# Kernel optimization log

Measured on AMD Instinct MI355X. Metric: run time of the kernel, lower is better.

## Reference

```python
import jax, jax.numpy as jnp
import numpy as np

NUM_FEATURES = 81   # atom feature width used in matmuls
N_NODES = 262144
N_COLS = 103        # num_features + num_bond
OUT_CH = 128
COORD = 3           # distance rule slice [0:3]


def setup_inputs() -> dict:
    key = jax.random.key(0)
    k1, k2, k3, k4 = jax.random.split(key, 4)
    features = jax.random.normal(k1, (N_NODES, N_COLS), dtype=jnp.float32)
    # columns 81, 82 hold neighbor indices (0 => no neighbor), stored as floats
    idx = jax.random.randint(k4, (N_NODES, 2), 0, N_NODES).astype(jnp.float32)
    features = features.at[:, NUM_FEATURES:NUM_FEATURES + 2].set(idx)
    w_s = jax.random.normal(k2, (NUM_FEATURES, OUT_CH), dtype=jnp.float32) * 0.05
    w_n = jax.random.normal(k3, (N_COLS, OUT_CH), dtype=jnp.float32) * 0.05
    return {"features": features, "w_s": w_s, "w_n": w_n}


def reference(features, w_s, w_n):
    F = NUM_FEATURES
    self_f = features[:, :F]                       # [N, F]
    new_features = self_f @ w_s                    # [N, C] self term

    idx0 = features[:, F].astype(jnp.int32)        # neighbor slot 0
    idx1 = features[:, F + 1].astype(jnp.int32)    # neighbor slot 1

    def neighbor_contrib(idx):
        nei = features[idx]                                        # gather [N, 103]
        # rule 0: 'distance' over [0:COORD] -> keep neighbor slice, record distance
        d = jnp.sqrt(jnp.sum(jnp.square(self_f[:, :COORD] - nei[:, :COORD]), axis=-1))
        seg_dist = nei[:, :COORD]                                  # [N, 3]
        # rule 1: 'sum' over [COORD:F]
        seg_sum = self_f[:, COORD:F] + nei[:, COORD:F]             # [N, F-3]
        comb = jnp.concatenate([seg_dist, seg_sum], axis=-1)       # [N, F]
        d_eff = jnp.where(d > 0, d, jnp.float32(0.01))
        comb = comb / jnp.square(d_eff)[:, None]                   # distance scaling
        return comb @ w_n[:F] + new_features                       # tiny-matmul batched

    c0 = neighbor_contrib(idx0)
    c1 = neighbor_contrib(idx1)
    # rows with no valid neighbor were never written -> zeros
    out = jnp.where((idx1 != 0)[:, None], c1,
                    jnp.where((idx0 != 0)[:, None], c0, jnp.float32(0.0)))
    return out
```

## Files before the change

### kernel.cpp

```cpp
#include <hip/hip_runtime.h>
#include <hip/hip_bf16.h>

constexpr int kNodes = 262144;
constexpr int NC  = 103;
constexpr int F   = 81;
constexpr int OC  = 128;
constexpr int NKS = 6;
constexpr int THREADS = 256;

typedef __attribute__((ext_vector_type(8))) short bf16x8;
typedef __attribute__((ext_vector_type(4))) float f32x4;

__device__ inline ushort f2bf(float f) {
  uint u = __float_as_uint(f);
  return (ushort)((u + 0x7fffu + ((u >> 16) & 1u)) >> 16);
}

__global__ __launch_bounds__(256)
void prep_w(const float* __restrict__ w_s, const float* __restrict__ w_n,
            ushort* __restrict__ wf) {
  int t = blockIdx.x * 256 + threadIdx.x;
  if (t >= NKS * 8 * 64) return;
  int l  = t & 63;
  int ct = (t >> 6) & 7;
  int ks = t >> 9;
  int c  = ct * 16 + (l & 15);
  int kb = ks * 32 + ((l >> 4) << 3);
  union { ushort u[8]; int4 v; } o;
  #pragma unroll
  for (int i = 0; i < 8; ++i) {
    int k = kb + i;
    float f = 0.f;
    if (k < F)                      f = w_s[k * OC + c];
    else if (k >= 96 && k < 96 + F) f = w_n[(k - 96) * OC + c];
    o.u[i] = f2bf(f);
  }
  ((int4*)wf)[t] = o.v;
}

__device__ inline short bfc(float x) {
  return (short)__bfloat16_as_ushort(__float2bfloat16(x));
}

__global__ __launch_bounds__(THREADS, 2)
void rgc_flat(const float* __restrict__ feat, const ushort* __restrict__ wf,
              float* __restrict__ out) {
  const int tid  = threadIdx.x;
  const int l    = tid & 63;
  const int q    = l >> 4;
  const int lrow = l & 15;
  const int off0 = q * 8;
  const long tbase = (long)(blockIdx.x * 4 + (tid >> 6)) * 16;
  const float* srow = feat + (tbase + lrow) * NC;
  const bf16x8* wfv = (const bf16x8*)wf;

  float pidx0 = srow[F];
  float pidx1 = srow[F + 1];
  float sc0 = srow[0], sc1 = srow[1], sc2 = srow[2];
  float s[24];
  #pragma unroll
  for (int c = 0; c < 3; ++c)
    #pragma unroll
    for (int i = 0; i < 8; ++i)
      s[c * 8 + i] = srow[c * 32 + off0 + i];

  bf16x8 bcur[8], bnxt[8];
  #pragma unroll
  for (int ct = 0; ct < 8; ++ct) bcur[ct] = wfv[ct * 64 + l];

  int i0 = (int)pidx0, i1 = (int)pidx1;
  int sel = (i1 != 0) ? i1 : i0;
  float alive = (i1 != 0 || i0 != 0) ? 1.f : 0.f;
  const float* nrow = feat + (long)sel * NC;
  float nc0 = nrow[0], nc1 = nrow[1], nc2 = nrow[2];
  float n[24];
  #pragma unroll
  for (int c = 0; c < 3; ++c)
    #pragma unroll
    for (int i = 0; i < 8; ++i)
      n[c * 8 + i] = nrow[c * 32 + off0 + i];

  float dx = sc0 - nc0, dy = sc1 - nc1, dz = sc2 - nc2;
  float d2 = dx * dx + dy * dy + dz * dz;
  float cs = alive * ((d2 > 0.f) ? (1.f / d2) : 10000.f);

  bf16x8 afS[3], afC[3];
  #pragma unroll
  for (int c = 0; c < 3; ++c) {
    #pragma unroll
    for (int i = 0; i < 8; ++i) {
      float sv = s[c * 8 + i];
      float nv = n[c * 8 + i];
      afS[c][i] = bfc(sv * alive);
      float se = sv;
      if (c == 0 && i < 3) se = (q == 0) ? 0.f : sv;
      afC[c][i] = bfc((nv + se) * cs);
    }
  }

  f32x4 acc[8];
  #pragma unroll
  for (int i = 0; i < 8; ++i) acc[i] = (f32x4)(0.f);

  #pragma unroll
  for (int ks = 0; ks < NKS; ++ks) {
    if (ks + 1 < NKS) {
      #pragma unroll
      for (int ct = 0; ct < 8; ++ct) bnxt[ct] = wfv[((ks + 1) * 8 + ct) * 64 + l];
    }
    bf16x8 af = (ks < 3) ? afS[ks] : afC[ks - 3];
    #pragma unroll
    for (int ct = 0; ct < 8; ++ct)
      acc[ct] = __builtin_amdgcn_mfma_f32_16x16x32_bf16(af, bcur[ct], acc[ct], 0, 0, 0);
    #pragma unroll
    for (int ct = 0; ct < 8; ++ct) bcur[ct] = bnxt[ct];
  }

  const long orow = tbase + q * 4;
  const int  col  = l & 15;
  #pragma unroll
  for (int ct = 0; ct < 8; ++ct) {
    #pragma unroll
    for (int r = 0; r < 4; ++r) {
      out[(orow + r) * OC + ct * 16 + col] = acc[ct][r];
    }
  }
}

extern "C" void kernel_launch(void* const* d_in, const int* in_sizes, int n_in,
                              void* d_out, int out_size, void* d_ws, size_t ws_size,
                              hipStream_t stream) {
  const float* feat = (const float*)d_in[0];
  const float* w_s  = (const float*)d_in[1];
  const float* w_n  = (const float*)d_in[2];
  float* outp = (float*)d_out;
  ushort* wf = (ushort*)d_ws;

  prep_w<<<dim3((NKS * 8 * 64 + 255) / 256), 256, 0, stream>>>(w_s, w_n, wf);
  rgc_flat<<<dim3(kNodes / 64), THREADS, 0, stream>>>(feat, wf, outp);
}
```

Measured before the change: 79.11 us.

## Process 32 rows per wave, reusing weight fragments across two row tiles

```diff
diff --git a/kernel.cpp b/kernel.cpp
--- a/kernel.cpp
+++ b/kernel.cpp
@@ -10,6 +10,7 @@
 
 typedef __attribute__((ext_vector_type(8))) short bf16x8;
 typedef __attribute__((ext_vector_type(4))) float f32x4;
+typedef __attribute__((ext_vector_type(8))) float f32x8;
 
 __device__ inline ushort f2bf(float f) {
   uint u = __float_as_uint(f);
@@ -42,87 +43,113 @@
   return (short)__bfloat16_as_ushort(__float2bfloat16(x));
 }
 
-__global__ __launch_bounds__(THREADS, 2)
-void rgc_flat(const float* __restrict__ feat, const ushort* __restrict__ wf,
-              float* __restrict__ out) {
+#define LOAD8(dst, p, base)                 \
+  {                                         \
+    _Pragma("unroll")                       \
+    for (int _i = 0; _i < 8; ++_i) (dst)[_i] = (p)[(base) + _i]; \
+  }
+
+__global__ __launch_bounds__(THREADS)
+void rgc_flat32(const float* __restrict__ feat, const ushort* __restrict__ wf,
+                float* __restrict__ out) {
   const int tid  = threadIdx.x;
   const int l    = tid & 63;
   const int q    = l >> 4;
   const int lrow = l & 15;
   const int off0 = q * 8;
-  const long tbase = (long)(blockIdx.x * 4 + (tid >> 6)) * 16;
-  const float* srow = feat + (tbase + lrow) * NC;
+  const long wbase = (long)(blockIdx.x * 4 + (tid >> 6)) * 32;
+  const float* srowA = feat + (wbase + lrow) * NC;
+  const float* srowB = feat + (wbase + 16 + lrow) * NC;
   const bf16x8* wfv = (const bf16x8*)wf;
 
-  float pidx0 = srow[F];
-  float pidx1 = srow[F + 1];
-  float sc0 = srow[0], sc1 = srow[1], sc2 = srow[2];
-  float s[24];
-  #pragma unroll
-  for (int c = 0; c < 3; ++c)
+  f32x8 vA0, vA1, vA2, vB0, vB1, vB2;
+  LOAD8(vA0, srowA, off0); LOAD8(vA1, srowA, 32 + off0); LOAD8(vA2, srowA, 64 + off0);
+  LOAD8(vB0, srowB, off0); LOAD8(vB1, srowB, 32 + off0); LOAD8(vB2, srowB, 64 + off0);
+  float iA0 = srowA[F], iA1 = srowA[F + 1];
+  float iB0 = srowB[F], iB1 = srowB[F + 1];
+  float cA0 = srowA[0], cA1 = srowA[1], cA2 = srowA[2];
+  float cB0 = srowB[0], cB1 = srowB[1], cB2 = srowB[2];
+  asm volatile("" :: "v"(vA0), "v"(vA1), "v"(vA2), "v"(vB0), "v"(vB1), "v"(vB2));
+
+  int selA; float aliveA;
+  { int i0 = (int)iA0, i1 = (int)iA1;
+    selA = (i1 != 0) ? i1 : i0; aliveA = (i1 != 0 || i0 != 0) ? 1.f : 0.f; }
+  int selB; float aliveB;
+  { int i0 = (int)iB0, i1 = (int)iB1;
+    selB = (i1 != 0) ? i1 : i0; aliveB = (i1 != 0 || i0 != 0) ? 1.f : 0.f; }
+  const float* nrowA = feat + (long)selA * NC;
+  const float* nrowB = feat + (long)selB * NC;
+
+  f32x8 wA0, wA1, wA2, wB0, wB1, wB2;
+  LOAD8(wA0, nrowA, off0); LOAD8(wA1, nrowA, 32 + off0); LOAD8(wA2, nrowA, 64 + off0);
+  LOAD8(wB0, nrowB, off0); LOAD8(wB1, nrowB, 32 + off0); LOAD8(wB2, nrowB, 64 + off0);
+  float nA0 = nrowA[0], nA1 = nrowA[1], nA2 = nrowA[2];
+  float nB0 = nrowB[0], nB1 = nrowB[1], nB2 = nrowB[2];
+  asm volatile("" :: "v"(wA0), "v"(wA1), "v"(wA2), "v"(wB0), "v"(wB1), "v"(wB2));
+
+  float dxA = cA0 - nA0, dyA = cA1 - nA1, dzA = cA2 - nA2;
+  float d2A = dxA * dxA + dyA * dyA + dzA * dzA;
+  float csA = aliveA * ((d2A > 0.f) ? (1.f / d2A) : 10000.f);
+  float dxB = cB0 - nB0, dyB = cB1 - nB1, dzB = cB2 - nB2;
+  float d2B = dxB * dxB + dyB * dyB + dzB * dzB;
+  float csB = aliveB * ((d2B > 0.f) ? (1.f / d2B) : 10000.f);
+
+  bf16x8 fSA[3], fCA[3], fSB[3], fCB[3];
+  {
+    const f32x8 sA[3] = {vA0, vA1, vA2}, sB[3] = {vB0, vB1, vB2};
+    const f32x8 nA[3] = {wA0, wA1, wA2}, nB[3] = {wB0, wB1, wB2};
     #pragma unroll
-    for (int i = 0; i < 8; ++i)
-      s[c * 8 + i] = srow[c * 32 + off0 + i];
-
-  bf16x8 bcur[8], bnxt[8];
-  #pragma unroll
-  for (int ct = 0; ct < 8; ++ct) bcur[ct] = wfv[ct * 64 + l];
-
-  int i0 = (int)pidx0, i1 = (int)pidx1;
-  int sel = (i1 != 0) ? i1 : i0;
-  float alive = (i1 != 0 || i0 != 0) ? 1.f : 0.f;
-  const float* nrow = feat + (long)sel * NC;
-  float nc0 = nrow[0], nc1 = nrow[1], nc2 = nrow[2];
-  float n[24];
-  #pragma unroll
-  for (int c = 0; c < 3; ++c)
-    #pragma unroll
-    for (int i = 0; i < 8; ++i)
-      n[c * 8 + i] = nrow[c * 32 + off0 + i];
-
-  float dx = sc0 - nc0, dy = sc1 - nc1, dz = sc2 - nc2;
-  float d2 = dx * dx + dy * dy + dz * dz;
-  float cs = alive * ((d2 > 0.f) ? (1.f / d2) : 10000.f);
-
-  bf16x8 afS[3], afC[3];
-  #pragma unroll
-  for (int c = 0; c < 3; ++c) {
-    #pragma unroll
-    for (int i = 0; i < 8; ++i) {
-      float sv = s[c * 8 + i];
-      float nv = n[c * 8 + i];
-      afS[c][i] = bfc(sv * alive);
-      float se = sv;
-      if (c == 0 && i < 3) se = (q == 0) ? 0.f : sv;
-      afC[c][i] = bfc((nv + se) * cs);
+    for (int c = 0; c < 3; ++c) {
+      #pragma unroll
+      for (int i = 0; i < 8; ++i) {
+        float svA = sA[c][i], nvA = nA[c][i];
+        float svB = sB[c][i], nvB = nB[c][i];
+        fSA[c][i] = bfc(svA * aliveA);
+        fSB[c][i] = bfc(svB * aliveB);
+        float seA = svA, seB = svB;
+        if (c == 0 && i < 3 && q == 0) { seA = 0.f; seB = 0.f; }
+        fCA[c][i] = bfc((nvA + seA) * csA);
+        fCB[c][i] = bfc((nvB + seB) * csB);
+      }
     }
   }
 
-  f32x4 acc[8];
+  const int col = l & 15;
   #pragma unroll
-  for (int i = 0; i < 8; ++i) acc[i] = (f32x4)(0.f);
+  for (int h = 0; h < 2; ++h) {
+    f32x4 accA[4], accB[4];
+    #pragma unroll
+    for (int j = 0; j < 4; ++j) { accA[j] = (f32x4)(0.f); accB[j] = (f32x4)(0.f); }
 
-  #pragma unroll
-  for (int ks = 0; ks < NKS; ++ks) {
-    if (ks + 1 < NKS) {
+    bf16x8 bc[4], bn[4];
+    #pragma unroll
+    for (int j = 0; j < 4; ++j) bc[j] = wfv[(h * 4 + j) * 64 + l];
+
+    #pragma unroll
+    for (int ks = 0; ks < NKS; ++ks) {
+      if (ks + 1 < NKS) {
+        #pragma unroll
+        for (int j = 0; j < 4; ++j) bn[j] = wfv[((ks + 1) * 8 + h * 4 + j) * 64 + l];
+      }
+      bf16x8 afA = (ks < 3) ? fSA[ks] : fCA[ks - 3];
+      bf16x8 afB = (ks < 3) ? fSB[ks] : fCB[ks - 3];
       #pragma unroll
-      for (int ct = 0; ct < 8; ++ct) bnxt[ct] = wfv[((ks + 1) * 8 + ct) * 64 + l];
+      for (int j = 0; j < 4; ++j) {
+        accA[j] = __builtin_amdgcn_mfma_f32_16x16x32_bf16(afA, bc[j], accA[j], 0, 0, 0);
+        accB[j] = __builtin_amdgcn_mfma_f32_16x16x32_bf16(afB, bc[j], accB[j], 0, 0, 0);
+      }
+      #pragma unroll
+      for (int j = 0; j < 4; ++j) bc[j] = bn[j];
     }
-    bf16x8 af = (ks < 3) ? afS[ks] : afC[ks - 3];
+
     #pragma unroll
-    for (int ct = 0; ct < 8; ++ct)
-      acc[ct] = __builtin_amdgcn_mfma_f32_16x16x32_bf16(af, bcur[ct], acc[ct], 0, 0, 0);
-    #pragma unroll
-    for (int ct = 0; ct < 8; ++ct) bcur[ct] = bnxt[ct];
-  }
-
-  const long orow = tbase + q * 4;
-  const int  col  = l & 15;
-  #pragma unroll
-  for (int ct = 0; ct < 8; ++ct) {
-    #pragma unroll
-    for (int r = 0; r < 4; ++r) {
-      out[(orow + r) * OC + ct * 16 + col] = acc[ct][r];
+    for (int j = 0; j < 4; ++j) {
+      const int ct = h * 4 + j;
+      #pragma unroll
+      for (int r = 0; r < 4; ++r) {
+        out[(wbase + q * 4 + r) * OC + ct * 16 + col]      = accA[j][r];
+        out[(wbase + 16 + q * 4 + r) * OC + ct * 16 + col] = accB[j][r];
+      }
     }
   }
 }
@@ -137,5 +164,5 @@
   ushort* wf = (ushort*)d_ws;
 
   prep_w<<<dim3((NKS * 8 * 64 + 255) / 256), 256, 0, stream>>>(w_s, w_n, wf);
-  rgc_flat<<<dim3(kNodes / 64), THREADS, 0, stream>>>(feat, wf, outp);
+  rgc_flat32<<<dim3(kNodes / 128), THREADS, 0, stream>>>(feat, wf, outp);
 }
```

Result: faster. 68.52 us (-13.4%).

## Stage self and neighbor rows in LDS with coalesced loads, split output columns across waves

Applied to the files above, without the earlier changes.

```diff
diff --git a/kernel.cpp b/kernel.cpp
--- a/kernel.cpp
+++ b/kernel.cpp
@@ -6,7 +6,10 @@
 constexpr int F   = 81;
 constexpr int OC  = 128;
 constexpr int NKS = 6;
+constexpr int NPB = 64;
 constexpr int THREADS = 256;
+constexpr int NEI_STRIDE = 100;
+constexpr int GW = 96;
 
 typedef __attribute__((ext_vector_type(8))) short bf16x8;
 typedef __attribute__((ext_vector_type(4))) float f32x4;
@@ -14,6 +17,10 @@
 __device__ inline ushort f2bf(float f) {
   uint u = __float_as_uint(f);
   return (ushort)((u + 0x7fffu + ((u >> 16) & 1u)) >> 16);
+}
+
+__device__ inline short bfc(float x) {
+  return (short)__bfloat16_as_ushort(__float2bfloat16(x));
 }
 
 __global__ __launch_bounds__(256)
@@ -38,91 +45,105 @@
   ((int4*)wf)[t] = o.v;
 }
 
-__device__ inline short bfc(float x) {
-  return (short)__bfloat16_as_ushort(__float2bfloat16(x));
-}
+__global__ __launch_bounds__(THREADS)
+void rgc_v8(const float* __restrict__ feat, const ushort* __restrict__ wf,
+            float* __restrict__ out) {
+  __shared__ float lds_self[NPB * NC];
+  __shared__ float lds_nei[NPB * NEI_STRIDE];
+  __shared__ int   s_sel[NPB];
+  __shared__ float s_alive[NPB];
+  __shared__ float s_cs[NPB];
 
-__global__ __launch_bounds__(THREADS, 2)
-void rgc_flat(const float* __restrict__ feat, const ushort* __restrict__ wf,
-              float* __restrict__ out) {
-  const int tid  = threadIdx.x;
-  const int l    = tid & 63;
+  const int tid = threadIdx.x;
+  const int w   = tid >> 6;
+  const int l   = tid & 63;
+  const long base = (long)blockIdx.x * NPB;
+  const float* fbase = feat + base * NC;
+
+  const bf16x8* wfv = (const bf16x8*)wf;
+  bf16x8 bA[NKS], bB[NKS];
+  #pragma unroll
+  for (int ks = 0; ks < NKS; ++ks) {
+    bA[ks] = wfv[(ks * 8 + w)     * 64 + l];
+    bB[ks] = wfv[(ks * 8 + w + 4) * 64 + l];
+  }
+
+  {
+    const float4* src = (const float4*)fbase;
+    float4* dst = (float4*)lds_self;
+    #pragma unroll
+    for (int i = tid; i < NPB * NC / 4; i += THREADS) dst[i] = src[i];
+  }
+  __syncthreads();
+
+  if (tid < NPB) {
+    int n = tid;
+    int i0 = (int)lds_self[n * NC + F];
+    int i1 = (int)lds_self[n * NC + F + 1];
+    s_sel[n]   = (i1 != 0) ? i1 : i0;
+    s_alive[n] = (i1 != 0 || i0 != 0) ? 1.f : 0.f;
+  }
+  __syncthreads();
+
+  #pragma unroll
+  for (int j = 0; j < 24; ++j) {
+    int v   = tid + j * THREADS;
+    int row = v / GW;
+    int col = v - row * GW;
+    lds_nei[row * NEI_STRIDE + col] = feat[(long)s_sel[row] * NC + col];
+  }
+  __syncthreads();
+
+  if (tid < NPB) {
+    int n = tid;
+    float dx = lds_self[n * NC + 0] - lds_nei[n * NEI_STRIDE + 0];
+    float dy = lds_self[n * NC + 1] - lds_nei[n * NEI_STRIDE + 1];
+    float dz = lds_self[n * NC + 2] - lds_nei[n * NEI_STRIDE + 2];
+    float d2 = dx * dx + dy * dy + dz * dz;
+    s_cs[n] = s_alive[n] * ((d2 > 0.f) ? (1.f / d2) : 10000.f);
+  }
+  __syncthreads();
+
   const int q    = l >> 4;
   const int lrow = l & 15;
   const int off0 = q * 8;
-  const long tbase = (long)(blockIdx.x * 4 + (tid >> 6)) * 16;
-  const float* srow = feat + (tbase + lrow) * NC;
-  const bf16x8* wfv = (const bf16x8*)wf;
-
-  float pidx0 = srow[F];
-  float pidx1 = srow[F + 1];
-  float sc0 = srow[0], sc1 = srow[1], sc2 = srow[2];
-  float s[24];
-  #pragma unroll
-  for (int c = 0; c < 3; ++c)
-    #pragma unroll
-    for (int i = 0; i < 8; ++i)
-      s[c * 8 + i] = srow[c * 32 + off0 + i];
-
-  bf16x8 bcur[8], bnxt[8];
-  #pragma unroll
-  for (int ct = 0; ct < 8; ++ct) bcur[ct] = wfv[ct * 64 + l];
-
-  int i0 = (int)pidx0, i1 = (int)pidx1;
-  int sel = (i1 != 0) ? i1 : i0;
-  float alive = (i1 != 0 || i0 != 0) ? 1.f : 0.f;
-  const float* nrow = feat + (long)sel * NC;
-  float nc0 = nrow[0], nc1 = nrow[1], nc2 = nrow[2];
-  float n[24];
-  #pragma unroll
-  for (int c = 0; c < 3; ++c)
-    #pragma unroll
-    for (int i = 0; i < 8; ++i)
-      n[c * 8 + i] = nrow[c * 32 + off0 + i];
-
-  float dx = sc0 - nc0, dy = sc1 - nc1, dz = sc2 - nc2;
-  float d2 = dx * dx + dy * dy + dz * dz;
-  float cs = alive * ((d2 > 0.f) ? (1.f / d2) : 10000.f);
-
-  bf16x8 afS[3], afC[3];
-  #pragma unroll
-  for (int c = 0; c < 3; ++c) {
-    #pragma unroll
-    for (int i = 0; i < 8; ++i) {
-      float sv = s[c * 8 + i];
-      float nv = n[c * 8 + i];
-      afS[c][i] = bfc(sv * alive);
-      float se = sv;
-      if (c == 0 && i < 3) se = (q == 0) ? 0.f : sv;
-      afC[c][i] = bfc((nv + se) * cs);
-    }
-  }
-
-  f32x4 acc[8];
-  #pragma unroll
-  for (int i = 0; i < 8; ++i) acc[i] = (f32x4)(0.f);
+  const int col  = l & 15;
 
   #pragma unroll
-  for (int ks = 0; ks < NKS; ++ks) {
-    if (ks + 1 < NKS) {
+  for (int nt = 0; nt < 4; ++nt) {
+    const int n = nt * 16 + lrow;
+    const float* sp = lds_self + n * NC;
+    const float* np = lds_nei + n * NEI_STRIDE;
+    const float alive = s_alive[n];
+    const float cs    = s_cs[n];
+
+    bf16x8 afS[3], afC[3];
+    #pragma unroll
+    for (int c = 0; c < 3; ++c) {
       #pragma unroll
-      for (int ct = 0; ct < 8; ++ct) bnxt[ct] = wfv[((ks + 1) * 8 + ct) * 64 + l];
+      for (int i = 0; i < 8; ++i) {
+        float sv = sp[c * 32 + off0 + i];
+        float nv = np[c * 32 + off0 + i];
+        afS[c][i] = bfc(sv * alive);
+        float se = sv;
+        if (c == 0 && i < 3 && q == 0) se = 0.f;
+        afC[c][i] = bfc((nv + se) * cs);
+      }
     }
-    bf16x8 af = (ks < 3) ? afS[ks] : afC[ks - 3];
+
+    f32x4 a0 = (f32x4)(0.f), a1 = (f32x4)(0.f);
     #pragma unroll
-    for (int ct = 0; ct < 8; ++ct)
-      acc[ct] = __builtin_amdgcn_mfma_f32_16x16x32_bf16(af, bcur[ct], acc[ct], 0, 0, 0);
-    #pragma unroll
-    for (int ct = 0; ct < 8; ++ct) bcur[ct] = bnxt[ct];
-  }
+    for (int ks = 0; ks < NKS; ++ks) {
+      bf16x8 af = (ks < 3) ? afS[ks] : afC[ks - 3];
+      a0 = __builtin_amdgcn_mfma_f32_16x16x32_bf16(af, bA[ks], a0, 0, 0, 0);
+      a1 = __builtin_amdgcn_mfma_f32_16x16x32_bf16(af, bB[ks], a1, 0, 0, 0);
+    }
 
-  const long orow = tbase + q * 4;
-  const int  col  = l & 15;
-  #pragma unroll
-  for (int ct = 0; ct < 8; ++ct) {
+    const long orow = base + nt * 16 + q * 4;
     #pragma unroll
     for (int r = 0; r < 4; ++r) {
-      out[(orow + r) * OC + ct * 16 + col] = acc[ct][r];
+      out[(orow + r) * OC + w * 16       + col] = a0[r];
+      out[(orow + r) * OC + (w + 4) * 16 + col] = a1[r];
     }
   }
 }
@@ -137,5 +158,5 @@
   ushort* wf = (ushort*)d_ws;
 
   prep_w<<<dim3((NKS * 8 * 64 + 255) / 256), 256, 0, stream>>>(w_s, w_n, wf);
-  rgc_flat<<<dim3(kNodes / 64), THREADS, 0, stream>>>(feat, wf, outp);
+  rgc_v8<<<dim3(kNodes / NPB), THREADS, 0, stream>>>(feat, wf, outp);
 }
```

Measured after the change: 67.91 us. 14.2% less time.
